# Optimization experiments

Measured on AMD Instinct MI355X. Metric: run time of the kernel, lower is better.

Reference implementation:

```python
import jax, jax.numpy as jnp
import numpy as np

B, T, D = 2, 2048, 2048
H, KV, HD = 16, 4, 128
EPS = 1e-6


def _rmsnorm(x, scale):
    # flax.linen.RMSNorm over last axis: x / sqrt(mean(x^2) + eps) * scale
    var = jnp.mean(jnp.square(x), axis=-1, keepdims=True)
    return x * jax.lax.rsqrt(var + EPS) * scale


def _rope(x, cos, sin):
    # x: [b, t, h, d]; cos/sin: [t, d]
    x_rot = jnp.stack([-x[..., 1::2], x[..., 0::2]], axis=-1)
    x_rot = x_rot.reshape(*x_rot.shape[:-2], -1)
    return x * cos[None, :, None, :] + x_rot * sin[None, :, None, :]


def setup_inputs() -> dict:
    key = jax.random.key(0)
    ks = jax.random.split(key, 5)
    x = jax.random.normal(ks[0], (B, T, D), jnp.float32)
    Wq = jax.random.normal(ks[1], (D, H * HD), jnp.float32) / np.sqrt(D)
    Wk = jax.random.normal(ks[2], (D, KV * HD), jnp.float32) / np.sqrt(D)
    Wv = jax.random.normal(ks[3], (D, KV * HD), jnp.float32) / np.sqrt(D)
    Wo = jax.random.normal(ks[4], (H * HD, D), jnp.float32) / np.sqrt(H * HD)
    q_scale = jnp.ones((HD,), jnp.float32)
    k_scale = jnp.ones((HD,), jnp.float32)
    # standard RoPE tables, interleaved-pair convention
    pos = jnp.arange(T, dtype=jnp.float32)
    inv_freq = 1.0 / (10000.0 ** (jnp.arange(0, HD, 2, dtype=jnp.float32) / HD))
    freqs = pos[:, None] * inv_freq[None, :]  # [T, HD/2]
    cos = jnp.repeat(jnp.cos(freqs), 2, axis=-1)  # [T, HD]
    sin = jnp.repeat(jnp.sin(freqs), 2, axis=-1)
    mask = jnp.tril(jnp.ones((T, T), bool))[None, None]  # causal [1,1,T,T]
    return {"x": x, "Wq": Wq, "Wk": Wk, "Wv": Wv, "Wo": Wo,
            "q_scale": q_scale, "k_scale": k_scale,
            "cos": cos, "sin": sin, "mask": mask}


def reference(x, Wq, Wk, Wv, Wo, q_scale, k_scale, cos, sin, mask):
    num_groups = H // KV
    q = (x @ Wq).reshape(B, T, H, HD)
    k = (x @ Wk).reshape(B, T, KV, HD)
    v = (x @ Wv).reshape(B, T, KV, HD)
    q = _rmsnorm(q, q_scale)
    k = _rmsnorm(k, k_scale)
    q = _rope(q, cos, sin)
    k = _rope(k, cos, sin)
    k = jnp.repeat(k, num_groups, axis=2)  # [b, t, H, d]
    v = jnp.repeat(v, num_groups, axis=2)
    scores = jnp.einsum('bqhd,bkhd->bhqk', q, k) / jnp.sqrt(jnp.float32(HD))
    scores = jnp.where(mask, scores, jnp.finfo(scores.dtype).min)
    attn = jax.nn.softmax(scores, axis=-1)
    out = jnp.einsum('bhqk,bkhd->bqhd', attn, v)
    out = out.reshape(B, T, H * HD)
    return out @ Wo
```

## Files before the change

kernel.cpp:

```cpp
#include <hip/hip_runtime.h>
#include <hip/hip_bf16.h>

#define B_   2
#define T_   2048
#define D_   2048
#define H_   16
#define KV_  4
#define HD_  128
#define BT_  (B_*T_)
#define QKVP 3072
#define KOFF 2048
#define VOFF 2560
static constexpr float EPS_ = 1e-6f;

typedef unsigned short u16;
typedef __attribute__((ext_vector_type(8))) short short8;
typedef __attribute__((ext_vector_type(4))) float f32x4;
typedef __attribute__((ext_vector_type(4))) unsigned short u16x4;

__device__ __forceinline__ u16 f2bf(float f){
    unsigned u = __float_as_uint(f);
    u += 0x7FFF + ((u >> 16) & 1);
    return (u16)(u >> 16);
}
__device__ __forceinline__ float bf2f(u16 u){
    return __uint_as_float((unsigned)u << 16);
}

__device__ __forceinline__ void async_copy16(const void* g, void* l) {
    __builtin_amdgcn_global_load_lds(
        (const __attribute__((address_space(1))) unsigned int*)g,
        (__attribute__((address_space(3))) unsigned int*)l, 16, 0, 0);
}

__global__ __launch_bounds__(256) void cvt_f32_bf16_kernel(
    const float* __restrict__ in, u16* __restrict__ out, int n)
{
    const int i = (blockIdx.x*256 + threadIdx.x)*4;
    if (i < n) {
        float4 v = *(const float4*)&in[i];
        u16x4 w = { f2bf(v.x), f2bf(v.y), f2bf(v.z), f2bf(v.w) };
        *(u16x4*)&out[i] = w;
    }
}

__global__ __launch_bounds__(256) void transpose_cvt_kernel(
    const float* __restrict__ in, u16* __restrict__ out, int R, int C)
{
    __shared__ u16 tile[64][65];
    const int r0 = blockIdx.y*64, c0 = blockIdx.x*64;
    const int tr = threadIdx.x >> 4;
    const int tc = (threadIdx.x & 15) * 4;
    #pragma unroll
    for (int i = 0; i < 4; i++) {
        const int r = tr + i*16;
        float4 v = *(const float4*)&in[(size_t)(r0 + r)*C + c0 + tc];
        tile[tc+0][r] = f2bf(v.x);
        tile[tc+1][r] = f2bf(v.y);
        tile[tc+2][r] = f2bf(v.z);
        tile[tc+3][r] = f2bf(v.w);
    }
    __syncthreads();
    #pragma unroll
    for (int i = 0; i < 4; i++) {
        const int c = tr + i*16;
        u16x4 w = { tile[c][tc+0], tile[c][tc+1], tile[c][tc+2], tile[c][tc+3] };
        *(u16x4*)&out[(size_t)(c0 + c)*R + r0 + tc] = w;
    }
}

__global__ __launch_bounds__(256) void transpose_v_kernel(
    const u16* __restrict__ qkv, u16* __restrict__ vt)
{
    __shared__ u16 tile[64][65];
    const int t0 = blockIdx.x*64;
    const int d0 = blockIdx.y*64;
    const int bk = blockIdx.z;
    const int tr = threadIdx.x >> 4;
    const int tc = (threadIdx.x & 15) * 4;
    #pragma unroll
    for (int i = 0; i < 4; i++) {
        const int t = t0 + tr + i*16;
        u16x4 v = *(const u16x4*)&qkv[(size_t)((bk>>2)*T_ + t)*QKVP + VOFF
                                      + (bk&3)*HD_ + d0 + tc];
        tile[tc+0][tr+i*16] = v[0];
        tile[tc+1][tr+i*16] = v[1];
        tile[tc+2][tr+i*16] = v[2];
        tile[tc+3][tr+i*16] = v[3];
    }
    __syncthreads();
    #pragma unroll
    for (int i = 0; i < 4; i++) {
        const int d = tr + i*16;
        u16x4 w = { tile[d][tc+0], tile[d][tc+1], tile[d][tc+2], tile[d][tc+3] };
        *(u16x4*)&vt[((size_t)bk*HD_ + d0 + d)*T_ + t0 + tc] = w;
    }
}

#define GBM 128
#define GBN 128
#define GBK 32

template<bool OUT_BF16>
__global__ __launch_bounds__(256) void gemm_mfma_kernel(
    const u16* __restrict__ A, const u16* __restrict__ Bt,
    void* __restrict__ C, int N, int K, int lda, int ldb, int ldc)
{
    __shared__ __align__(16) u16 As[GBM][GBK];
    __shared__ __align__(16) u16 Bs[GBN][GBK];
    const int tid  = threadIdx.x;
    const int lane = tid & 63;
    const int wave = tid >> 6;
    const int l15  = lane & 15;
    const int quad = lane >> 4;
    const int wr   = (wave >> 1) * 64;
    const int wc   = (wave & 1) * 64;
    const size_t row0 = (size_t)blockIdx.y * GBM;
    const size_t col0 = (size_t)blockIdx.x * GBN;

    f32x4 acc[4][4];
    #pragma unroll
    for (int i = 0; i < 4; i++)
        #pragma unroll
        for (int j = 0; j < 4; j++)
            acc[i][j] = (f32x4){0.f,0.f,0.f,0.f};

    for (int k0 = 0; k0 < K; k0 += GBK) {
        #pragma unroll
        for (int c = 0; c < 2; c++) {
            const int e = (c*256 + tid) * 8;
            const int r = e >> 5, cc = e & 31;
            async_copy16(A  + (row0 + r)*lda + k0 + cc, &As[r][cc]);
            async_copy16(Bt + (col0 + r)*ldb + k0 + cc, &Bs[r][cc]);
        }
        __syncthreads();

        short8 af[4], bf[4];
        #pragma unroll
        for (int i = 0; i < 4; i++)
            af[i] = *(const short8*)&As[wr + i*16 + l15][quad*8];
        #pragma unroll
        for (int j = 0; j < 4; j++)
            bf[j] = *(const short8*)&Bs[wc + j*16 + l15][quad*8];
        #pragma unroll
        for (int i = 0; i < 4; i++)
            #pragma unroll
            for (int j = 0; j < 4; j++)
                acc[i][j] = __builtin_amdgcn_mfma_f32_16x16x32_bf16(
                    af[i], bf[j], acc[i][j], 0, 0, 0);
        __syncthreads();
    }

    #pragma unroll
    for (int i = 0; i < 4; i++)
        #pragma unroll
        for (int r = 0; r < 4; r++) {
            const size_t row = row0 + wr + i*16 + quad*4 + r;
            #pragma unroll
            for (int j = 0; j < 4; j++) {
                const size_t col = col0 + wc + j*16 + l15;
                if (OUT_BF16) ((u16*)C)[row*ldc + col] = f2bf(acc[i][j][r]);
                else          ((float*)C)[row*ldc + col] = acc[i][j][r];
            }
        }
}

__global__ __launch_bounds__(256) void rmsnorm_rope_kernel(
    u16* __restrict__ qk, const float* __restrict__ scale,
    const float* __restrict__ cosT, const float* __restrict__ sinT,
    int heads_per_token, int head_off, float post_scale)
{
    const int wid   = blockIdx.x*4 + (threadIdx.x >> 6);
    const int lane  = threadIdx.x & 63;
    const int token = wid / heads_per_token;
    const int hidx  = wid % heads_per_token;
    const int t     = token & (T_ - 1);
    u16* p = qk + (size_t)token*QKVP + head_off + hidx*HD_ + lane*2;

    const unsigned u = *(const unsigned*)p;
    const float x0 = bf2f((u16)(u & 0xffff));
    const float x1 = bf2f((u16)(u >> 16));
    float ss = x0*x0 + x1*x1;
    #pragma unroll
    for (int off = 32; off > 0; off >>= 1) ss += __shfl_xor(ss, off);
    const float rms = rsqrtf(ss * (1.0f/HD_) + EPS_);

    const float2 sc = *(const float2*)&scale[lane*2];
    const float2 cs = *(const float2*)&cosT[(size_t)t*HD_ + lane*2];
    const float2 sn = *(const float2*)&sinT[(size_t)t*HD_ + lane*2];
    const float n0 = x0 * rms * sc.x;
    const float n1 = x1 * rms * sc.y;
    const float r0 = (n0*cs.x - n1*sn.x) * post_scale;
    const float r1 = (n1*cs.y + n0*sn.y) * post_scale;
    *(unsigned*)p = (unsigned)f2bf(r0) | ((unsigned)f2bf(r1) << 16);
}

#define BQ  64
#define BKV 64

__global__ __launch_bounds__(256, 4) void attn_mfma9_kernel(
    const u16* __restrict__ qkv, const u16* __restrict__ Vtg)
{
    __shared__ __align__(16) u16 Ks[16][BKV][8];
    __shared__ __align__(16) u16 Vt[8][HD_][8];
    __shared__ __align__(16) u16 Pb[4][8][16][8];

    const int n   = blockIdx.x + 32*blockIdx.y + 512*blockIdx.z;
    const int s   = n >> 8;
    const int x   = n & 31;
    const int y0  = (n >> 5) & 7;
    const int qt  = (s & 1) ? x : 31 - x;
    const int h   = y0 + 8*(s & 1);
    const int b   = s >> 1;

    const int kvh  = h >> 2;
    const int tid  = threadIdx.x;
    const int lane = tid & 63;
    const int wave = tid >> 6;
    const int l15  = lane & 15;
    const int quad = lane >> 4;
    const int q0   = qt * BQ;

    short8 qf[4];
    {
        const u16* qbase = qkv + (size_t)(b*T_ + q0 + wave*16 + l15)*QKVP + h*HD_;
        #pragma unroll
        for (int kt = 0; kt < 4; kt++)
            qf[kt] = *(const short8*)(qbase + (kt*4 + quad)*8);
    }

    float lsum[4] = {0.f, 0.f, 0.f, 0.f};
    f32x4 oacc[8];
    #pragma unroll
    for (int cv = 0; cv < 8; cv++) oacc[cv] = (f32x4){0.f,0.f,0.f,0.f};

    const int ntiles = qt + 1;
    for (int t = 0; t < ntiles; t++) {
        const int k0 = t * BKV;
        __syncthreads();

        #pragma unroll
        for (int it = 0; it < 4; it++) {
            const int n2  = it*256 + tid;
            const int cc  = n2 >> 6;
            const int key = n2 & 63;
            async_copy16(qkv + (size_t)(b*T_ + k0 + key)*QKVP + KOFF + kvh*HD_ + cc*8,
                         &Ks[cc][key][0]);
        }
        #pragma unroll
        for (int it = 0; it < 4; it++) {
            const int n2 = it*256 + tid;
            const int cc = n2 >> 7;
            const int d  = n2 & 127;
            async_copy16(Vtg + ((size_t)(b*KV_ + kvh)*HD_ + d)*T_ + k0 + cc*8,
                         &Vt[cc][d][0]);
        }
        __syncthreads();

        f32x4 s4[4];
        #pragma unroll
        for (int c = 0; c < 4; c++) s4[c] = (f32x4){0.f,0.f,0.f,0.f};
        __builtin_amdgcn_s_setprio(1);
        #pragma unroll
        for (int kt = 0; kt < 4; kt++) {
            #pragma unroll
            for (int c = 0; c < 4; c++) {
                short8 bf = *(const short8*)&Ks[kt*4 + quad][c*16 + l15][0];
                s4[c] = __builtin_amdgcn_mfma_f32_16x16x32_bf16(qf[kt], bf, s4[c], 0, 0, 0);
            }
        }
        __builtin_amdgcn_s_setprio(0);

        if (t == ntiles - 1) {
            const int qrow0 = q0 + wave*16 + quad*4;
            #pragma unroll
            for (int r = 0; r < 4; r++)
                #pragma unroll
                for (int c = 0; c < 4; c++) {
                    const int key = k0 + c*16 + l15;
                    if (key > qrow0 + r) s4[c][r] = -1e30f;
                }
        }
        #pragma unroll
        for (int r = 0; r < 4; r++)
            #pragma unroll
            for (int c = 0; c < 4; c++) {
                const float p = __expf(s4[c][r]);
                s4[c][r] = p;
                lsum[r] += p;
            }

        #pragma unroll
        for (int r = 0; r < 4; r++)
            #pragma unroll
            for (int c = 0; c < 4; c++)
                Pb[wave][c*2 + (l15 >> 3)][quad*4 + r][l15 & 7] = f2bf(s4[c][r]);

        __builtin_amdgcn_s_setprio(1);
        #pragma unroll
        for (int kt2 = 0; kt2 < 2; kt2++) {
            short8 a = *(const short8*)&Pb[wave][kt2*4 + quad][l15][0];
            #pragma unroll
            for (int cv = 0; cv < 8; cv++) {
                short8 vf = *(const short8*)&Vt[kt2*4 + quad][cv*16 + l15][0];
                oacc[cv] = __builtin_amdgcn_mfma_f32_16x16x32_bf16(a, vf, oacc[cv], 0, 0, 0);
            }
        }
        __builtin_amdgcn_s_setprio(0);
    }

    #pragma unroll
    for (int r = 0; r < 4; r++) {
        float tot = lsum[r];
        #pragma unroll
        for (int off = 1; off < 16; off <<= 1)
            tot += __shfl_xor(tot, off, 16);
        const float linv = 1.0f / tot;
        u16* orow = (u16*)qkv + (size_t)(b*T_ + q0 + wave*16 + quad*4 + r)*QKVP
                    + h*HD_ + l15;
        #pragma unroll
        for (int cv = 0; cv < 8; cv++)
            orow[cv*16] = f2bf(oacc[cv][r] * linv);
    }
}

extern "C" void kernel_launch(void* const* d_in, const int* in_sizes, int n_in,
                              void* d_out, int out_size, void* d_ws, size_t ws_size,
                              hipStream_t stream)
{
    const float* x    = (const float*)d_in[0];
    const float* Wq   = (const float*)d_in[1];
    const float* Wk   = (const float*)d_in[2];
    const float* Wv   = (const float*)d_in[3];
    const float* Wo   = (const float*)d_in[4];
    const float* qsc  = (const float*)d_in[5];
    const float* ksc  = (const float*)d_in[6];
    const float* cosT = (const float*)d_in[7];
    const float* sinT = (const float*)d_in[8];
    float* out = (float*)d_out;

    u16* xb     = (u16*)d_ws;
    u16* Wqkvt  = xb    + (size_t)BT_*D_;
    u16* Wot    = Wqkvt + (size_t)QKVP*D_;
    u16* qkv    = Wot   + (size_t)D_*(H_*HD_);
    u16* vtg    = qkv   + (size_t)BT_*QKVP;

    cvt_f32_bf16_kernel<<<(BT_*D_)/1024, 256, 0, stream>>>(x, xb, BT_*D_);
    transpose_cvt_kernel<<<dim3((H_*HD_)/64,  D_/64), 256, 0, stream>>>(
        Wq, Wqkvt, D_, H_*HD_);
    transpose_cvt_kernel<<<dim3((KV_*HD_)/64, D_/64), 256, 0, stream>>>(
        Wk, Wqkvt + (size_t)KOFF*D_, D_, KV_*HD_);
    transpose_cvt_kernel<<<dim3((KV_*HD_)/64, D_/64), 256, 0, stream>>>(
        Wv, Wqkvt + (size_t)VOFF*D_, D_, KV_*HD_);
    transpose_cvt_kernel<<<dim3(D_/64, (H_*HD_)/64),  256, 0, stream>>>(
        Wo, Wot, H_*HD_, D_);

    gemm_mfma_kernel<true><<<dim3(QKVP/GBN, BT_/GBM), 256, 0, stream>>>(
        xb, Wqkvt, qkv, QKVP, D_, D_, D_, QKVP);

    rmsnorm_rope_kernel<<<(BT_*H_)/4,  256, 0, stream>>>(
        qkv, qsc, cosT, sinT, H_, 0, 0.08838834764831845f);
    rmsnorm_rope_kernel<<<(BT_*KV_)/4, 256, 0, stream>>>(
        qkv, ksc, cosT, sinT, KV_, KOFF, 1.0f);

    transpose_v_kernel<<<dim3(T_/64, HD_/64, B_*KV_), 256, 0, stream>>>(qkv, vtg);

    attn_mfma9_kernel<<<dim3(T_/BQ, H_, B_), 256, 0, stream>>>(qkv, vtg);

    gemm_mfma_kernel<false><<<dim3(D_/GBN, BT_/GBM), 256, 0, stream>>>(
        qkv, Wot, out, D_, D_, QKVP, D_, D_);
}
```

Baseline: 379.1 us.

## Split long causal query tiles across two blocks and merge partials

Query tiles 19 and above split their key range into two halves, each handled by its own block. Each half writes unnormalized fp32 partial outputs and row sums to a buffer in the workspace region that is dead by then, and a new combine kernel adds the halves and normalizes. The aim is to shorten the longest causal blocks so the grid's critical path and load imbalance shrink. The cost is an extra launch and the fp32 partial writes and reads. The heavy-first block ordering is replaced by a simpler grid where split blocks come first.

New measurement: 398.7 us. 5.2% more time.

```diff
diff --git a/kernel.cpp b/kernel.cpp
--- a/kernel.cpp
+++ b/kernel.cpp
@@ -197,22 +197,38 @@
 
 #define BQ  64
 #define BKV 64
-
-__global__ __launch_bounds__(256, 4) void attn_mfma9_kernel(
-    const u16* __restrict__ qkv, const u16* __restrict__ Vtg)
+#define QT_SPLIT 19
+#define NSPLIT   (32 - QT_SPLIT)
+#define PSLOT    16512
+#define PHALF    8256
+
+__global__ __launch_bounds__(256, 4) void attn_mfma10_kernel(
+    const u16* __restrict__ qkv, const u16* __restrict__ Vtg,
+    float* __restrict__ part)
 {
     __shared__ __align__(16) u16 Ks[16][BKV][8];
     __shared__ __align__(16) u16 Vt[8][HD_][8];
     __shared__ __align__(16) u16 Pb[4][8][16][8];
 
-    const int n   = blockIdx.x + 32*blockIdx.y + 512*blockIdx.z;
-    const int s   = n >> 8;
-    const int x   = n & 31;
-    const int y0  = (n >> 5) & 7;
-    const int qt  = (s & 1) ? x : 31 - x;
-    const int h   = y0 + 8*(s & 1);
-    const int b   = s >> 1;
-
+    const int m = blockIdx.x;
+    int qt, t0, t1, half;
+    bool full;
+    if (m < 2*NSPLIT) {
+        qt = 31 - (m >> 1);
+        const int cnt = qt + 1;
+        const int kA  = cnt - (cnt >> 1);
+        half = m & 1;
+        t0 = half ? kA : 0;
+        t1 = half ? cnt : kA;
+        full = false;
+    } else {
+        qt = 18 - (m - 2*NSPLIT);
+        t0 = 0; t1 = qt + 1; half = 0;
+        full = true;
+    }
+
+    const int h    = blockIdx.y;
+    const int b    = blockIdx.z;
     const int kvh  = h >> 2;
     const int tid  = threadIdx.x;
     const int lane = tid & 63;
@@ -234,8 +250,7 @@
     #pragma unroll
     for (int cv = 0; cv < 8; cv++) oacc[cv] = (f32x4){0.f,0.f,0.f,0.f};
 
-    const int ntiles = qt + 1;
-    for (int t = 0; t < ntiles; t++) {
+    for (int t = t0; t < t1; t++) {
         const int k0 = t * BKV;
         __syncthreads();
 
@@ -271,7 +286,7 @@
         }
         __builtin_amdgcn_s_setprio(0);
 
-        if (t == ntiles - 1) {
+        if (t == qt) {
             const int qrow0 = q0 + wave*16 + quad*4;
             #pragma unroll
             for (int r = 0; r < 4; r++)
@@ -309,18 +324,61 @@
         __builtin_amdgcn_s_setprio(0);
     }
 
-    #pragma unroll
-    for (int r = 0; r < 4; r++) {
-        float tot = lsum[r];
-        #pragma unroll
-        for (int off = 1; off < 16; off <<= 1)
-            tot += __shfl_xor(tot, off, 16);
-        const float linv = 1.0f / tot;
-        u16* orow = (u16*)qkv + (size_t)(b*T_ + q0 + wave*16 + quad*4 + r)*QKVP
-                    + h*HD_ + l15;
-        #pragma unroll
-        for (int cv = 0; cv < 8; cv++)
-            orow[cv*16] = f2bf(oacc[cv][r] * linv);
+    if (full) {
+        #pragma unroll
+        for (int r = 0; r < 4; r++) {
+            float tot = lsum[r];
+            #pragma unroll
+            for (int off = 1; off < 16; off <<= 1)
+                tot += __shfl_xor(tot, off, 16);
+            const float linv = 1.0f / tot;
+            u16* orow = (u16*)qkv + (size_t)(b*T_ + q0 + wave*16 + quad*4 + r)*QKVP
+                        + h*HD_ + l15;
+            #pragma unroll
+            for (int cv = 0; cv < 8; cv++)
+                orow[cv*16] = f2bf(oacc[cv][r] * linv);
+        }
+    } else {
+        float* po = part + (size_t)((b*H_ + h)*NSPLIT + (qt - QT_SPLIT))*PSLOT
+                         + (size_t)half*PHALF;
+        #pragma unroll
+        for (int r = 0; r < 4; r++) {
+            float tot = lsum[r];
+            #pragma unroll
+            for (int off = 1; off < 16; off <<= 1)
+                tot += __shfl_xor(tot, off, 16);
+            const int row = wave*16 + quad*4 + r;
+            #pragma unroll
+            for (int cv = 0; cv < 8; cv++)
+                po[row*128 + cv*16 + l15] = oacc[cv][r];
+            if (l15 == 0) po[8192 + row] = tot;
+        }
+    }
+}
+
+__global__ __launch_bounds__(256) void attn_combine_kernel(
+    const float* __restrict__ part, u16* __restrict__ qkv)
+{
+    const int p  = blockIdx.x;
+    const int qt = QT_SPLIT + (p % NSPLIT);
+    const int bh = p / NSPLIT;
+    const int h  = bh & 15;
+    const int b  = bh >> 4;
+    const float* p0 = part + (size_t)p*PSLOT;
+    const float* p1 = p0 + PHALF;
+    const int tid = threadIdx.x;
+    const int row = tid >> 2;
+    const int c0  = (tid & 3) * 32;
+    const float linv = 1.0f / (p0[8192 + row] + p1[8192 + row]);
+    u16* orow = qkv + (size_t)(b*T_ + qt*BQ + row)*QKVP + h*HD_;
+    #pragma unroll
+    for (int d = 0; d < 32; d += 4) {
+        const int col = c0 + d;
+        u16x4 w = { f2bf((p0[row*128 + col+0] + p1[row*128 + col+0]) * linv),
+                    f2bf((p0[row*128 + col+1] + p1[row*128 + col+1]) * linv),
+                    f2bf((p0[row*128 + col+2] + p1[row*128 + col+2]) * linv),
+                    f2bf((p0[row*128 + col+3] + p1[row*128 + col+3]) * linv) };
+        *(u16x4*)&orow[col] = w;
     }
 }
 
@@ -344,6 +402,7 @@
     u16* Wot    = Wqkvt + (size_t)QKVP*D_;
     u16* qkv    = Wot   + (size_t)D_*(H_*HD_);
     u16* vtg    = qkv   + (size_t)BT_*QKVP;
+    float* part = (float*)d_ws;
 
     cvt_f32_bf16_kernel<<<(BT_*D_)/1024, 256, 0, stream>>>(x, xb, BT_*D_);
     transpose_cvt_kernel<<<dim3((H_*HD_)/64,  D_/64), 256, 0, stream>>>(
@@ -365,7 +424,10 @@
 
     transpose_v_kernel<<<dim3(T_/64, HD_/64, B_*KV_), 256, 0, stream>>>(qkv, vtg);
 
-    attn_mfma9_kernel<<<dim3(T_/BQ, H_, B_), 256, 0, stream>>>(qkv, vtg);
+    attn_mfma10_kernel<<<dim3(19 + 2*NSPLIT, H_, B_), 256, 0, stream>>>(
+        qkv, vtg, part);
+
+    attn_combine_kernel<<<B_*H_*NSPLIT, 256, 0, stream>>>(part, qkv);
 
     gemm_mfma_kernel<false><<<dim3(D_/GBN, BT_/GBM), 256, 0, stream>>>(
         qkv, Wot, out, D_, D_, QKVP, D_, D_);
```
